# Optimization experiments

Measured on AMD Instinct MI355X. Metric: run time of the kernel, lower is better.

The kernel has to match this reference:

```python
import jax, jax.numpy as jnp
import numpy as np


def setup_inputs() -> dict:
    key = jax.random.key(0)
    ks = jax.random.split(key, 7)
    B, T, DIN, D = 64, 512, 512, 512
    s_in = 1.0 / np.sqrt(DIN)  # ~glorot-ish scale for input kernels
    s_h = 1.0 / np.sqrt(D)     # scale for recurrent kernels (orthogonal-ish magnitude)
    return {
        "X": jax.random.normal(ks[0], (B, T, DIN), jnp.float32),
        "W_z": jax.random.normal(ks[1], (DIN, D), jnp.float32) * s_in,
        "U_z": jax.random.normal(ks[2], (D, D), jnp.float32) * s_h,
        "b_z": jnp.zeros((D,), jnp.float32),
        "W_r": jax.random.normal(ks[3], (DIN, D), jnp.float32) * s_in,
        "U_r": jax.random.normal(ks[4], (D, D), jnp.float32) * s_h,
        "b_r": jnp.zeros((D,), jnp.float32),
        "W_h": jax.random.normal(ks[5], (DIN, D), jnp.float32) * s_in,
        "U_h": jax.random.normal(ks[6], (D, D), jnp.float32) * s_h,
        "b_h": jnp.zeros((D,), jnp.float32),
        "mask": jnp.ones((B, T), jnp.int32),
    }


def reference(X, W_z, U_z, b_z, W_r, U_r, b_r, W_h, U_h, b_h, mask):
    # X: [B, T, DIN] -> time-major [T, B, DIN]
    Xt = jnp.transpose(X, (1, 0, 2))
    # Precompute input projections (large GEMMs, done once): [T, B, D]
    xz = Xt @ W_z + b_z
    xr = Xt @ W_r + b_r
    xh = Xt @ W_h + b_h
    # Padded/shifted mask (pad=1): step t sees mask[t-1]; step 0 sees 0,
    # which zeroes the (zero) initial state exactly as in the theano code.
    m = jnp.transpose(mask, (1, 0)).astype(X.dtype)[:, :, None]  # [T, B, 1]
    m_tm1 = jnp.concatenate([jnp.zeros_like(m[:1]), m[:-1]], axis=0)

    B = X.shape[0]
    D = W_z.shape[1]
    h0 = jnp.zeros((B, D), X.dtype)

    def step(h_tm1, inputs):
        xz_t, xr_t, xh_t, mt = inputs
        hm = mt * h_tm1                                  # masked previous state
        z = jax.nn.sigmoid(xz_t + hm @ U_z)              # update gate
        r = jax.nn.sigmoid(xr_t + hm @ U_r)              # reset gate
        hh = jnp.tanh(xh_t + (r * hm) @ U_h)             # candidate
        h_t = z * hm + (1.0 - z) * hh
        return h_t, None

    h_last, _ = jax.lax.scan(step, h0, (xz, xr, xh, m_tm1))
    # return_sequences=False -> last hidden state [B, D]
    return h_last
```

## Files before the change

kernel.cpp:

```cpp
#include <hip/hip_runtime.h>
#include <hip/hip_fp16.h>

#define B_   64
#define T_   512
#define DINc 512
#define D_   512
#define NWG  16
#define JS   32

typedef _Float16 half8 __attribute__((ext_vector_type(8)));
typedef _Float16 half4 __attribute__((ext_vector_type(4)));
typedef float   floatx4 __attribute__((ext_vector_type(4)));
typedef unsigned uintx4 __attribute__((ext_vector_type(4)));

__global__ __launch_bounds__(256) void k_cvtX(const float* __restrict__ X, _Float16* __restrict__ Xh) {
    int idx = blockIdx.x * 256 + threadIdx.x;
    int m  = idx >> 6;
    int k8 = idx & 63;
    int b = m & 63, t = m >> 6;
    const float* src = X + ((size_t)(b * T_ + t)) * DINc + k8 * 8;
    float4 f0 = *(const float4*)(src);
    float4 f1 = *(const float4*)(src + 4);
    half8 h;
    h[0] = (_Float16)f0.x; h[1] = (_Float16)f0.y; h[2] = (_Float16)f0.z; h[3] = (_Float16)f0.w;
    h[4] = (_Float16)f1.x; h[5] = (_Float16)f1.y; h[6] = (_Float16)f1.z; h[7] = (_Float16)f1.w;
    *(half8*)(Xh + (size_t)m * DINc + k8 * 8) = h;
}

__global__ __launch_bounds__(256) void k_cvtW(const float* __restrict__ M0, const float* __restrict__ M1,
                                              const float* __restrict__ M2, _Float16* __restrict__ Mt) {
    __shared__ float tile[64][65];
    int g = blockIdx.z;
    const float* W = (g == 0) ? M0 : ((g == 1) ? M1 : M2);
    int n0 = blockIdx.x * 64, k0 = blockIdx.y * 64;
    int c = threadIdx.x & 63, r4 = threadIdx.x >> 6;
#pragma unroll
    for (int i = 0; i < 16; ++i) {
        int k = r4 + i * 4;
        tile[k][c] = W[(size_t)(k0 + k) * D_ + n0 + c];
    }
    __syncthreads();
    _Float16* out = Mt + (size_t)g * D_ * DINc;
#pragma unroll
    for (int i = 0; i < 16; ++i) {
        int n = r4 + i * 4;
        out[(size_t)(n0 + n) * DINc + k0 + c] = (_Float16)tile[c][n];
    }
}

__global__ __launch_bounds__(256) void k_cvtM(const int* __restrict__ mask, float* __restrict__ maskT) {
    int idx = blockIdx.x * 256 + threadIdx.x;
    int t = idx >> 6, b = idx & 63;
    maskT[idx] = (float)mask[(size_t)b * T_ + t];
}

__global__ __launch_bounds__(256) void k_gemm(const _Float16* __restrict__ Xh, const _Float16* __restrict__ Wt,
                                              const float* __restrict__ bz, const float* __restrict__ br,
                                              const float* __restrict__ bh, _Float16* __restrict__ xprojT) {
    __shared__ _Float16 As[128 * 32];
    __shared__ _Float16 Bs[128 * 32];
    int g = blockIdx.z;
    const _Float16* Wg = Wt + (size_t)g * 512 * 512;
    const float* bias = (g == 0) ? bz : ((g == 1) ? br : bh);
    _Float16* out = xprojT + (size_t)g * 16777216;
    int mb = blockIdx.x * 128, nb = blockIdx.y * 128;
    int tid = threadIdx.x, l = tid & 63, w = tid >> 6;
    int wr = w >> 1, wc = w & 1;
    int lr = l & 15, lg = l >> 4;

    floatx4 acc[4][4] = {};

    int ga0 = tid, ga1 = tid + 256;
    int ra0 = ga0 >> 2, ca0 = (ga0 & 3) * 8;
    int ra1 = ga1 >> 2, ca1 = (ga1 & 3) * 8;

    uint4 pa0, pa1, pb0, pb1;
    pa0 = *(const uint4*)(Xh + (size_t)(mb + ra0) * 512 + ca0);
    pa1 = *(const uint4*)(Xh + (size_t)(mb + ra1) * 512 + ca1);
    pb0 = *(const uint4*)(Wg + (size_t)(nb + ra0) * 512 + ca0);
    pb1 = *(const uint4*)(Wg + (size_t)(nb + ra1) * 512 + ca1);

    for (int kt = 0; kt < 16; ++kt) {
        __syncthreads();
        *(uint4*)(&As[ga0 * 8]) = pa0;
        *(uint4*)(&As[ga1 * 8]) = pa1;
        *(uint4*)(&Bs[ga0 * 8]) = pb0;
        *(uint4*)(&Bs[ga1 * 8]) = pb1;
        __syncthreads();
        if (kt < 15) {
            int kb = (kt + 1) * 32;
            pa0 = *(const uint4*)(Xh + (size_t)(mb + ra0) * 512 + kb + ca0);
            pa1 = *(const uint4*)(Xh + (size_t)(mb + ra1) * 512 + kb + ca1);
            pb0 = *(const uint4*)(Wg + (size_t)(nb + ra0) * 512 + kb + ca0);
            pb1 = *(const uint4*)(Wg + (size_t)(nb + ra1) * 512 + kb + ca1);
        }
        half8 af[4], bf[4];
#pragma unroll
        for (int mi = 0; mi < 4; mi++) af[mi] = *(const half8*)(&As[(wr * 64 + mi * 16 + lr) * 32 + lg * 8]);
#pragma unroll
        for (int ni = 0; ni < 4; ni++) bf[ni] = *(const half8*)(&Bs[(wc * 64 + ni * 16 + lr) * 32 + lg * 8]);
#pragma unroll
        for (int mi = 0; mi < 4; mi++)
#pragma unroll
            for (int ni = 0; ni < 4; ni++)
                acc[mi][ni] = __builtin_amdgcn_mfma_f32_16x16x32_f16(af[mi], bf[ni], acc[mi][ni], 0, 0, 0);
    }

#pragma unroll
    for (int ni = 0; ni < 4; ni++) {
        int col = nb + wc * 64 + ni * 16 + lr;
        float bv = bias[col];
#pragma unroll
        for (int mi = 0; mi < 4; mi++) {
            int row = mb + wr * 64 + mi * 16 + lg * 4;
            int tt = row >> 6, bb = row & 63;
            half4 hv;
#pragma unroll
            for (int i = 0; i < 4; i++) hv[i] = (_Float16)(acc[mi][ni][i] + bv);
            *(half4*)(out + (size_t)tt * 32768 + (size_t)col * 64 + bb) = hv;
        }
    }
}

__device__ __forceinline__ void st_agent(unsigned long long* p, unsigned long long v) {
    __hip_atomic_store(p, v, __ATOMIC_RELAXED, __HIP_MEMORY_SCOPE_AGENT);
}
__device__ __forceinline__ unsigned ld_flag(const unsigned* p) {
    return __hip_atomic_load(p, __ATOMIC_RELAXED, __HIP_MEMORY_SCOPE_AGENT);
}
__device__ __forceinline__ void st_flag(unsigned* p, unsigned v) {
    __hip_atomic_store(p, v, __ATOMIC_RELAXED, __HIP_MEMORY_SCOPE_AGENT);
}
__device__ __forceinline__ uintx4 ld16_agent(const void* p) {
    uintx4 r;
    asm volatile("global_load_dwordx4 %0, %1, off sc0 sc1" : "=v"(r) : "v"(p) : "memory");
    return r;
}

__device__ __forceinline__ unsigned long long pack_quad(const float v4[4], int lr) {
    unsigned long long unit = 0;
    int j = lr & 3;
#pragma unroll
    for (int i = 0; i < 4; i++) {
        _Float16 hv = (_Float16)v4[i];
        unsigned int v = (unsigned int)__builtin_bit_cast(unsigned short, hv);
        unsigned int o1 = __shfl_xor(v, 1, 64);
        unsigned int pair = (lr & 1) ? (o1 | (v << 16)) : (v | (o1 << 16));
        unsigned int q2 = __shfl_xor(pair, 2, 64);
        unsigned long long u = (lr & 2) ? ((unsigned long long)q2 | ((unsigned long long)pair << 32))
                                        : ((unsigned long long)pair | ((unsigned long long)q2 << 32));
        if (i == j) unit = u;
    }
    return unit;
}

__global__ __launch_bounds__(512, 2) void k_scan(const _Float16* __restrict__ Ut,
                                                 const float* __restrict__ maskT,
                                                 const _Float16* __restrict__ xprojT,
                                                 unsigned long long* __restrict__ hbuf,
                                                 unsigned long long* __restrict__ rhbuf,
                                                 unsigned* __restrict__ fh, unsigned* __restrict__ fr,
                                                 float* __restrict__ out) {
    __shared__ __align__(16) _Float16 Ulds[2 * JS * 512];
    __shared__ __align__(16) _Float16 Stg[64 * 512];
    char* StgB = (char*)Stg;
    int tid = threadIdx.x, l = tid & 63, w = tid >> 6;
    int lr = l & 15, lg = l >> 4;
    int mt = w >> 1, nt = w & 1;
    int slot = blockIdx.x;
    int jsb = slot * JS;

    for (int c = tid; c < 2 * JS * 64; c += 512) {
        int g  = c >> 11;
        int n  = (c >> 6) & 31;
        int k16 = c & 63;
        uintx4 v = *(const uintx4*)(Ut + (size_t)g * 262144 + (size_t)(jsb + n) * 512 + k16 * 8);
        *(uintx4*)((char*)Ulds + g * 32768 + n * 1024 + ((k16 * 16) ^ ((n & 7) << 4))) = v;
    }
    half8 uhf[16];
    {
        const _Float16* UtH = Ut + (size_t)2 * 262144;
        int ncol = jsb + nt * 16 + lr;
#pragma unroll
        for (int j = 0; j < 16; j++)
            uhf[j] = *(const half8*)(UtH + (size_t)ncol * 512 + j * 32 + lg * 8);
    }
    __syncthreads();

    const char* UB = (const char*)Ulds + (nt * 16 + lr) * 1024;
    const int swz = (lr & 7) << 4;

    int row0 = mt * 16 + lg * 4;
    int colg = jsb + nt * 16 + lr;

    float h4[4]  = {0.f, 0.f, 0.f, 0.f};
    float hm4[4] = {0.f, 0.f, 0.f, 0.f};

    const int punit = (mt * 16 + lg * 4 + (lr & 3)) * 128 + ((jsb + nt * 16) >> 2) + ((lr >> 2) & 3);
    const char* SB = StgB + (mt * 16 + lr) * 1024;

    const _Float16* xzB = xprojT + (size_t)colg * 64 + row0;
    const _Float16* xrB = xzB + (size_t)16777216;
    const _Float16* xhB = xrB + (size_t)16777216;

    {
        half4 xz0 = *(const half4*)(xzB);
        half4 xh0 = *(const half4*)(xhB);
        float4 m0 = *(const float4*)(maskT + row0);
#pragma unroll
        for (int i = 0; i < 4; i++) {
            float z  = 1.f / (1.f + __expf(-(float)xz0[i]));
            float hh = tanhf((float)xh0[i]);
            h4[i]  = (1.f - z) * hh;
            hm4[i] = ((float)m0[i]) * h4[i];
        }
        st_agent(hbuf + punit, pack_quad(hm4, lr));
        asm volatile("s_waitcnt vmcnt(0)" ::: "memory");
        __syncthreads();
        if (tid == 0) st_flag(fh + slot * 16, 1u);
    }

    for (int t = 1; t < T_; ++t) {
        const char* hmG = (const char*)(hbuf + ((t - 1) & 1) * 8192);
        char*       rhG = (char*)(rhbuf + (t & 1) * 8192);
        unsigned long long* rhW = rhbuf + (t & 1) * 8192;
        unsigned long long* hW  = hbuf + (t & 1) * 8192;

        half4 xzp = *(const half4*)(xzB + (size_t)t * 32768);
        half4 xrp = *(const half4*)(xrB + (size_t)t * 32768);
        half4 xhp = *(const half4*)(xhB + (size_t)t * 32768);
        float4 mv = *(const float4*)(maskT + (size_t)t * 64 + row0);

        if (w == 0) {
            for (;;) {
                unsigned v = (l < NWG) ? ld_flag(fh + l * 16) : (unsigned)t;
                if (__all(v >= (unsigned)t)) break;
            }
        }
        __syncthreads();
        {
            uintx4 gg[8];
#pragma unroll
            for (int it = 0; it < 8; ++it)
                gg[it] = ld16_agent(hmG + (w * 8 + it) * 1024 + l * 16);
            asm volatile("s_waitcnt vmcnt(0)" ::: "memory");
#pragma unroll
            for (int it = 0; it < 8; ++it)
                *(uintx4*)(StgB + (w * 8 + it) * 1024 + ((l * 16) ^ (it << 4))) = gg[it];
        }
        __syncthreads();
        half8 af[16];
#pragma unroll
        for (int j = 0; j < 16; j++)
            af[j] = *(const half8*)(SB + ((j * 64 + lg * 16) ^ swz));
        floatx4 accz = {0.f, 0.f, 0.f, 0.f}, accr = {0.f, 0.f, 0.f, 0.f};
#pragma unroll
        for (int j = 0; j < 16; j++) {
            int boff = (j * 64 + lg * 16) ^ swz;
            half8 bz8 = *(const half8*)(UB + boff);
            half8 br8 = *(const half8*)(UB + 32768 + boff);
            accz = __builtin_amdgcn_mfma_f32_16x16x32_f16(af[j], bz8, accz, 0, 0, 0);
            accr = __builtin_amdgcn_mfma_f32_16x16x32_f16(af[j], br8, accr, 0, 0, 0);
        }
        float z4[4], rh4[4];
#pragma unroll
        for (int i = 0; i < 4; i++) {
            float zz = 1.f / (1.f + __expf(-((float)xzp[i] + accz[i])));
            float rr = 1.f / (1.f + __expf(-((float)xrp[i] + accr[i])));
            z4[i]  = zz;
            rh4[i] = rr * hm4[i];
        }
        st_agent(rhW + punit, pack_quad(rh4, lr));
        asm volatile("s_waitcnt vmcnt(0)" ::: "memory");
        __syncthreads();
        if (tid == 0) st_flag(fr + slot * 16, (unsigned)t);

        if (w == 0) {
            for (;;) {
                unsigned v = (l < NWG) ? ld_flag(fr + l * 16) : (unsigned)t;
                if (__all(v >= (unsigned)t)) break;
            }
        }
        __syncthreads();
        {
            uintx4 gg[8];
#pragma unroll
            for (int it = 0; it < 8; ++it)
                gg[it] = ld16_agent(rhG + (w * 8 + it) * 1024 + l * 16);
            asm volatile("s_waitcnt vmcnt(0)" ::: "memory");
#pragma unroll
            for (int it = 0; it < 8; ++it)
                *(uintx4*)(StgB + (w * 8 + it) * 1024 + ((l * 16) ^ (it << 4))) = gg[it];
        }
        __syncthreads();
        half8 af2[16];
#pragma unroll
        for (int j = 0; j < 16; j++)
            af2[j] = *(const half8*)(SB + ((j * 64 + lg * 16) ^ swz));
        floatx4 acch0 = {0.f, 0.f, 0.f, 0.f}, acch1 = {0.f, 0.f, 0.f, 0.f};
#pragma unroll
        for (int j = 0; j < 16; j += 2) {
            acch0 = __builtin_amdgcn_mfma_f32_16x16x32_f16(af2[j],     uhf[j],     acch0, 0, 0, 0);
            acch1 = __builtin_amdgcn_mfma_f32_16x16x32_f16(af2[j + 1], uhf[j + 1], acch1, 0, 0, 0);
        }
#pragma unroll
        for (int i = 0; i < 4; i++) {
            float hh = tanhf((float)xhp[i] + acch0[i] + acch1[i]);
            h4[i]  = z4[i] * hm4[i] + (1.f - z4[i]) * hh;
            hm4[i] = ((float)mv[i]) * h4[i];
        }
        st_agent(hW + punit, pack_quad(hm4, lr));
        asm volatile("s_waitcnt vmcnt(0)" ::: "memory");
        __syncthreads();
        if (tid == 0) st_flag(fh + slot * 16, (unsigned)(t + 1));
    }

#pragma unroll
    for (int i = 0; i < 4; i++)
        out[(size_t)(row0 + i) * 512 + colg] = h4[i];
}

extern "C" void kernel_launch(void* const* d_in, const int* in_sizes, int n_in,
                              void* d_out, int out_size, void* d_ws, size_t ws_size,
                              hipStream_t stream) {
    (void)in_sizes; (void)n_in; (void)out_size; (void)ws_size;
    const float* X  = (const float*)d_in[0];
    const float* Wz = (const float*)d_in[1];
    const float* Uz = (const float*)d_in[2];
    const float* bz = (const float*)d_in[3];
    const float* Wr = (const float*)d_in[4];
    const float* Ur = (const float*)d_in[5];
    const float* br = (const float*)d_in[6];
    const float* Wh = (const float*)d_in[7];
    const float* Uh = (const float*)d_in[8];
    const float* bh = (const float*)d_in[9];
    const int* mask = (const int*)d_in[10];
    float* out = (float*)d_out;

    char* ws = (char*)d_ws;
    unsigned* fh = (unsigned*)ws;
    unsigned* fr = (unsigned*)(ws + 1024);
    unsigned long long* hbuf  = (unsigned long long*)(ws + 8192);
    unsigned long long* rhbuf = (unsigned long long*)(ws + 8192 + 131072);
    _Float16* Xh     = (_Float16*)(ws + 8192 + 2 * 131072);
    _Float16* Wt     = (_Float16*)(ws + 8192 + 2 * 131072 + 33554432);
    _Float16* Ut     = (_Float16*)(ws + 8192 + 2 * 131072 + 33554432 + 1572864);
    _Float16* xprojT = (_Float16*)(ws + 8192 + 2 * 131072 + 33554432 + 2 * 1572864);
    float*    maskT  = (float*)(ws + 8192 + 2 * 131072 + 33554432 + 2 * 1572864 + 100663296);

    hipMemsetAsync(ws, 0, 8192, stream);
    hipLaunchKernelGGL(k_cvtX, dim3(8192), dim3(256), 0, stream, X, Xh);
    hipLaunchKernelGGL(k_cvtW, dim3(8, 8, 3), dim3(256), 0, stream, Wz, Wr, Wh, Wt);
    hipLaunchKernelGGL(k_cvtW, dim3(8, 8, 3), dim3(256), 0, stream, Uz, Ur, Uh, Ut);
    hipLaunchKernelGGL(k_cvtM, dim3(128), dim3(256), 0, stream, mask, maskT);
    hipLaunchKernelGGL(k_gemm, dim3(256, 4, 3), dim3(256), 0, stream, Xh, Wt, bz, br, bh, xprojT);
    hipLaunchKernelGGL(k_scan, dim3(NWG), dim3(512), 0, stream, Ut, maskT, xprojT,
                       hbuf, rhbuf, fh, fr, out);
}
```

Before: 4.307 ms.

## Halve scan workgroups to 8 with 64 columns each and split-K staging

```diff
diff --git a/kernel.cpp b/kernel.cpp
--- a/kernel.cpp
+++ b/kernel.cpp
@@ -5,13 +5,18 @@
 #define T_   512
 #define DINc 512
 #define D_   512
-#define NWG  16
-#define JS   32
+#define NWG  8
+#define JS   64
 
 typedef _Float16 half8 __attribute__((ext_vector_type(8)));
 typedef _Float16 half4 __attribute__((ext_vector_type(4)));
 typedef float   floatx4 __attribute__((ext_vector_type(4)));
 typedef unsigned uintx4 __attribute__((ext_vector_type(4)));
+
+#define WAITV(N) asm volatile("s_waitcnt vmcnt(" #N ")" ::: "memory")
+#define WAITL()  asm volatile("s_waitcnt lgkmcnt(0)" ::: "memory")
+#define SCB()    __builtin_amdgcn_sched_barrier(0)
+#define RBAR()   do { SCB(); __builtin_amdgcn_s_barrier(); SCB(); } while (0)
 
 __global__ __launch_bounds__(256) void k_cvtX(const float* __restrict__ X, _Float16* __restrict__ Xh) {
     int idx = blockIdx.x * 256 + threadIdx.x;
@@ -154,28 +159,30 @@
     return unit;
 }
 
-__global__ __launch_bounds__(512, 2) void k_scan(const _Float16* __restrict__ Ut,
-                                                 const float* __restrict__ maskT,
-                                                 const _Float16* __restrict__ xprojT,
-                                                 unsigned long long* __restrict__ hbuf,
-                                                 unsigned long long* __restrict__ rhbuf,
-                                                 unsigned* __restrict__ fh, unsigned* __restrict__ fr,
-                                                 float* __restrict__ out) {
-    __shared__ __align__(16) _Float16 Ulds[2 * JS * 512];
-    __shared__ __align__(16) _Float16 Stg[64 * 512];
-    char* StgB = (char*)Stg;
+__global__ __launch_bounds__(512) void k_scan(const _Float16* __restrict__ Ut,
+                                              const float* __restrict__ maskT,
+                                              const _Float16* __restrict__ xprojT,
+                                              unsigned long long* __restrict__ hbuf,
+                                              unsigned long long* __restrict__ rhbuf,
+                                              unsigned* __restrict__ fh, unsigned* __restrict__ fr,
+                                              float* __restrict__ out) {
+    __shared__ __align__(16) char Lds[163840];
+    char* LdsB = Lds;
+    char* StgB = Lds + 131072;
     int tid = threadIdx.x, l = tid & 63, w = tid >> 6;
     int lr = l & 15, lg = l >> 4;
-    int mt = w >> 1, nt = w & 1;
+    int nt  = w >> 1;
+    int mt2 = w & 1;
+    int m0 = mt2 * 16, m1 = m0 + 32;
     int slot = blockIdx.x;
     int jsb = slot * JS;
 
-    for (int c = tid; c < 2 * JS * 64; c += 512) {
-        int g  = c >> 11;
-        int n  = (c >> 6) & 31;
+    for (int c = tid; c < 2 * 64 * 64; c += 512) {
+        int g   = c >> 12;
+        int n   = (c >> 6) & 63;
         int k16 = c & 63;
         uintx4 v = *(const uintx4*)(Ut + (size_t)g * 262144 + (size_t)(jsb + n) * 512 + k16 * 8);
-        *(uintx4*)((char*)Ulds + g * 32768 + n * 1024 + ((k16 * 16) ^ ((n & 7) << 4))) = v;
+        *(uintx4*)(LdsB + g * 65536 + n * 1024 + ((k16 * 16) ^ ((n & 7) << 4))) = v;
     }
     half8 uhf[16];
     {
@@ -187,49 +194,63 @@
     }
     __syncthreads();
 
-    const char* UB = (const char*)Ulds + (nt * 16 + lr) * 1024;
+    const char* UBz = LdsB + (nt * 16 + lr) * 1024;
+    const char* UBr = UBz + 65536;
     const int swz = (lr & 7) << 4;
-
-    int row0 = mt * 16 + lg * 4;
+    const int r0s = (m0 + lr) * 512;
+    const int r1s = (m1 + lr) * 512;
+
     int colg = jsb + nt * 16 + lr;
-
-    float h4[4]  = {0.f, 0.f, 0.f, 0.f};
-    float hm4[4] = {0.f, 0.f, 0.f, 0.f};
-
-    const int punit = (mt * 16 + lg * 4 + (lr & 3)) * 128 + ((jsb + nt * 16) >> 2) + ((lr >> 2) & 3);
-    const char* SB = StgB + (mt * 16 + lr) * 1024;
-
-    const _Float16* xzB = xprojT + (size_t)colg * 64 + row0;
+    int row0 = m0 + lg * 4;
+    int row1 = m1 + lg * 4;
+
+    float h4[2][4]  = {};
+    float hm4[2][4] = {};
+
+    const int punit0 = (m0 + lg * 4 + (lr & 3)) * 128 + ((jsb + nt * 16) >> 2) + ((lr >> 2) & 3);
+    const int punit1 = (m1 + lg * 4 + (lr & 3)) * 128 + ((jsb + nt * 16) >> 2) + ((lr >> 2) & 3);
+
+    const int gr0  = w * 8 + (l >> 5);
+    const int gcol = (l & 31) * 16;
+
+    const _Float16* xzB = xprojT + (size_t)colg * 64;
     const _Float16* xrB = xzB + (size_t)16777216;
     const _Float16* xhB = xrB + (size_t)16777216;
 
     {
-        half4 xz0 = *(const half4*)(xzB);
-        half4 xh0 = *(const half4*)(xhB);
-        float4 m0 = *(const float4*)(maskT + row0);
+        half4 xz0a = *(const half4*)(xzB + row0), xz0b = *(const half4*)(xzB + row1);
+        half4 xh0a = *(const half4*)(xhB + row0), xh0b = *(const half4*)(xhB + row1);
+        float4 m0a = *(const float4*)(maskT + row0), m0b = *(const float4*)(maskT + row1);
 #pragma unroll
         for (int i = 0; i < 4; i++) {
-            float z  = 1.f / (1.f + __expf(-(float)xz0[i]));
-            float hh = tanhf((float)xh0[i]);
-            h4[i]  = (1.f - z) * hh;
-            hm4[i] = ((float)m0[i]) * h4[i];
-        }
-        st_agent(hbuf + punit, pack_quad(hm4, lr));
-        asm volatile("s_waitcnt vmcnt(0)" ::: "memory");
+            float za = 1.f / (1.f + __expf(-(float)xz0a[i]));
+            float zb = 1.f / (1.f + __expf(-(float)xz0b[i]));
+            h4[0][i] = (1.f - za) * tanhf((float)xh0a[i]);
+            h4[1][i] = (1.f - zb) * tanhf((float)xh0b[i]);
+            hm4[0][i] = ((float)m0a[i]) * h4[0][i];
+            hm4[1][i] = ((float)m0b[i]) * h4[1][i];
+        }
+        st_agent(hbuf + punit0, pack_quad(hm4[0], lr));
+        st_agent(hbuf + punit1, pack_quad(hm4[1], lr));
+        WAITV(0);
         __syncthreads();
         if (tid == 0) st_flag(fh + slot * 16, 1u);
     }
 
     for (int t = 1; t < T_; ++t) {
         const char* hmG = (const char*)(hbuf + ((t - 1) & 1) * 8192);
-        char*       rhG = (char*)(rhbuf + (t & 1) * 8192);
+        const char* rhG = (const char*)(rhbuf + (t & 1) * 8192);
         unsigned long long* rhW = rhbuf + (t & 1) * 8192;
         unsigned long long* hW  = hbuf + (t & 1) * 8192;
 
-        half4 xzp = *(const half4*)(xzB + (size_t)t * 32768);
-        half4 xrp = *(const half4*)(xrB + (size_t)t * 32768);
-        half4 xhp = *(const half4*)(xhB + (size_t)t * 32768);
-        float4 mv = *(const float4*)(maskT + (size_t)t * 64 + row0);
+        const _Float16* xzT = xzB + (size_t)t * 32768;
+        const _Float16* xrT = xrB + (size_t)t * 32768;
+        const _Float16* xhT = xhB + (size_t)t * 32768;
+        half4 xzp0 = *(const half4*)(xzT + row0), xzp1 = *(const half4*)(xzT + row1);
+        half4 xrp0 = *(const half4*)(xrT + row0), xrp1 = *(const half4*)(xrT + row1);
+        half4 xhp0 = *(const half4*)(xhT + row0), xhp1 = *(const half4*)(xhT + row1);
+        float4 mva = *(const float4*)(maskT + (size_t)t * 64 + row0);
+        float4 mvb = *(const float4*)(maskT + (size_t)t * 64 + row1);
 
         if (w == 0) {
             for (;;) {
@@ -238,40 +259,69 @@
             }
         }
         __syncthreads();
+
+        floatx4 accz0 = {}, accz1 = {}, accr0 = {}, accr1 = {};
         {
             uintx4 gg[8];
 #pragma unroll
-            for (int it = 0; it < 8; ++it)
-                gg[it] = ld16_agent(hmG + (w * 8 + it) * 1024 + l * 16);
-            asm volatile("s_waitcnt vmcnt(0)" ::: "memory");
-#pragma unroll
-            for (int it = 0; it < 8; ++it)
-                *(uintx4*)(StgB + (w * 8 + it) * 1024 + ((l * 16) ^ (it << 4))) = gg[it];
-        }
-        __syncthreads();
-        half8 af[16];
-#pragma unroll
-        for (int j = 0; j < 16; j++)
-            af[j] = *(const half8*)(SB + ((j * 64 + lg * 16) ^ swz));
-        floatx4 accz = {0.f, 0.f, 0.f, 0.f}, accr = {0.f, 0.f, 0.f, 0.f};
-#pragma unroll
-        for (int j = 0; j < 16; j++) {
-            int boff = (j * 64 + lg * 16) ^ swz;
-            half8 bz8 = *(const half8*)(UB + boff);
-            half8 br8 = *(const half8*)(UB + 32768 + boff);
-            accz = __builtin_amdgcn_mfma_f32_16x16x32_f16(af[j], bz8, accz, 0, 0, 0);
-            accr = __builtin_amdgcn_mfma_f32_16x16x32_f16(af[j], br8, accr, 0, 0, 0);
-        }
-        float z4[4], rh4[4];
+            for (int it = 0; it < 4; ++it)
+                gg[it] = ld16_agent(hmG + (gr0 + it * 2) * 1024 + gcol);
+#pragma unroll
+            for (int it = 0; it < 4; ++it)
+                gg[4 + it] = ld16_agent(hmG + (gr0 + it * 2) * 1024 + 512 + gcol);
+            WAITV(4); SCB();
+#pragma unroll
+            for (int it = 0; it < 4; ++it) {
+                int r = gr0 + it * 2;
+                *(uintx4*)(StgB + r * 512 + (gcol ^ ((r & 7) << 4))) = gg[it];
+            }
+            WAITL(); RBAR();
+#pragma unroll
+            for (int j = 0; j < 8; ++j) {
+                int kbyte = j * 64 + lg * 16;
+                half8 a0 = *(const half8*)(StgB + r0s + (kbyte ^ swz));
+                half8 a1 = *(const half8*)(StgB + r1s + (kbyte ^ swz));
+                int ub = kbyte ^ swz;
+                half8 bz = *(const half8*)(UBz + ub);
+                half8 br = *(const half8*)(UBr + ub);
+                accz0 = __builtin_amdgcn_mfma_f32_16x16x32_f16(a0, bz, accz0, 0, 0, 0);
+                accr0 = __builtin_amdgcn_mfma_f32_16x16x32_f16(a0, br, accr0, 0, 0, 0);
+                accz1 = __builtin_amdgcn_mfma_f32_16x16x32_f16(a1, bz, accz1, 0, 0, 0);
+                accr1 = __builtin_amdgcn_mfma_f32_16x16x32_f16(a1, br, accr1, 0, 0, 0);
+            }
+            RBAR();
+            WAITV(0); SCB();
+#pragma unroll
+            for (int it = 0; it < 4; ++it) {
+                int r = gr0 + it * 2;
+                *(uintx4*)(StgB + r * 512 + (gcol ^ ((r & 7) << 4))) = gg[4 + it];
+            }
+            WAITL(); RBAR();
+#pragma unroll
+            for (int j = 0; j < 8; ++j) {
+                int kbyte = j * 64 + lg * 16;
+                half8 a0 = *(const half8*)(StgB + r0s + (kbyte ^ swz));
+                half8 a1 = *(const half8*)(StgB + r1s + (kbyte ^ swz));
+                int ub = (512 + kbyte) ^ swz;
+                half8 bz = *(const half8*)(UBz + ub);
+                half8 br = *(const half8*)(UBr + ub);
+                accz0 = __builtin_amdgcn_mfma_f32_16x16x32_f16(a0, bz, accz0, 0, 0, 0);
+                accr0 = __builtin_amdgcn_mfma_f32_16x16x32_f16(a0, br, accr0, 0, 0, 0);
+                accz1 = __builtin_amdgcn_mfma_f32_16x16x32_f16(a1, bz, accz1, 0, 0, 0);
+                accr1 = __builtin_amdgcn_mfma_f32_16x16x32_f16(a1, br, accr1, 0, 0, 0);
+            }
+        }
+        float z4[2][4], rh4[2][4];
 #pragma unroll
         for (int i = 0; i < 4; i++) {
-            float zz = 1.f / (1.f + __expf(-((float)xzp[i] + accz[i])));
-            float rr = 1.f / (1.f + __expf(-((float)xrp[i] + accr[i])));
-            z4[i]  = zz;
-            rh4[i] = rr * hm4[i];
-        }
-        st_agent(rhW + punit, pack_quad(rh4, lr));
-        asm volatile("s_waitcnt vmcnt(0)" ::: "memory");
+            z4[0][i] = 1.f / (1.f + __expf(-((float)xzp0[i] + accz0[i])));
+            z4[1][i] = 1.f / (1.f + __expf(-((float)xzp1[i] + accz1[i])));
+            rh4[0][i] = (1.f / (1.f + __expf(-((float)xrp0[i] + accr0[i])))) * hm4[0][i];
+            rh4[1][i] = (1.f / (1.f + __expf(-((float)xrp1[i] + accr1[i])))) * hm4[1][i];
+        }
+        st_agent(rhW + punit0, pack_quad(rh4[0], lr));
+        st_agent(rhW + punit1, pack_quad(rh4[1], lr));
+        WAITV(0);
         __syncthreads();
         if (tid == 0) st_flag(fr + slot * 16, (unsigned)t);
 
@@ -282,42 +332,69 @@
             }
         }
         __syncthreads();
+
+        floatx4 acch0 = {}, acch1 = {};
         {
             uintx4 gg[8];
 #pragma unroll
-            for (int it = 0; it < 8; ++it)
-                gg[it] = ld16_agent(rhG + (w * 8 + it) * 1024 + l * 16);
-            asm volatile("s_waitcnt vmcnt(0)" ::: "memory");
-#pragma unroll
-            for (int it = 0; it < 8; ++it)
-                *(uintx4*)(StgB + (w * 8 + it) * 1024 + ((l * 16) ^ (it << 4))) = gg[it];
-        }
-        __syncthreads();
-        half8 af2[16];
-#pragma unroll
-        for (int j = 0; j < 16; j++)
-            af2[j] = *(const half8*)(SB + ((j * 64 + lg * 16) ^ swz));
-        floatx4 acch0 = {0.f, 0.f, 0.f, 0.f}, acch1 = {0.f, 0.f, 0.f, 0.f};
-#pragma unroll
-        for (int j = 0; j < 16; j += 2) {
-            acch0 = __builtin_amdgcn_mfma_f32_16x16x32_f16(af2[j],     uhf[j],     acch0, 0, 0, 0);
-            acch1 = __builtin_amdgcn_mfma_f32_16x16x32_f16(af2[j + 1], uhf[j + 1], acch1, 0, 0, 0);
+            for (int it = 0; it < 4; ++it)
+                gg[it] = ld16_agent(rhG + (gr0 + it * 2) * 1024 + gcol);
+#pragma unroll
+            for (int it = 0; it < 4; ++it)
+                gg[4 + it] = ld16_agent(rhG + (gr0 + it * 2) * 1024 + 512 + gcol);
+            WAITV(4); SCB();
+#pragma unroll
+            for (int it = 0; it < 4; ++it) {
+                int r = gr0 + it * 2;
+                *(uintx4*)(StgB + r * 512 + (gcol ^ ((r & 7) << 4))) = gg[it];
+            }
+            WAITL(); RBAR();
+#pragma unroll
+            for (int j = 0; j < 8; ++j) {
+                int kbyte = j * 64 + lg * 16;
+                half8 a0 = *(const half8*)(StgB + r0s + (kbyte ^ swz));
+                half8 a1 = *(const half8*)(StgB + r1s + (kbyte ^ swz));
+                acch0 = __builtin_amdgcn_mfma_f32_16x16x32_f16(a0, uhf[j], acch0, 0, 0, 0);
+                acch1 = __builtin_amdgcn_mfma_f32_16x16x32_f16(a1, uhf[j], acch1, 0, 0, 0);
+            }
+            RBAR();
+            WAITV(0); SCB();
+#pragma unroll
+            for (int it = 0; it < 4; ++it) {
+                int r = gr0 + it * 2;
+                *(uintx4*)(StgB + r * 512 + (gcol ^ ((r & 7) << 4))) = gg[4 + it];
+            }
+            WAITL(); RBAR();
+#pragma unroll
+            for (int j = 0; j < 8; ++j) {
+                int kbyte = j * 64 + lg * 16;
+                half8 a0 = *(const half8*)(StgB + r0s + (kbyte ^ swz));
+                half8 a1 = *(const half8*)(StgB + r1s + (kbyte ^ swz));
+                acch0 = __builtin_amdgcn_mfma_f32_16x16x32_f16(a0, uhf[8 + j], acch0, 0, 0, 0);
+                acch1 = __builtin_amdgcn_mfma_f32_16x16x32_f16(a1, uhf[8 + j], acch1, 0, 0, 0);
+            }
         }
 #pragma unroll
         for (int i = 0; i < 4; i++) {
-            float hh = tanhf((float)xhp[i] + acch0[i] + acch1[i]);
-            h4[i]  = z4[i] * hm4[i] + (1.f - z4[i]) * hh;
-            hm4[i] = ((float)mv[i]) * h4[i];
-        }
-        st_agent(hW + punit, pack_quad(hm4, lr));
-        asm volatile("s_waitcnt vmcnt(0)" ::: "memory");
+            float hha = tanhf((float)xhp0[i] + acch0[i]);
+            float hhb = tanhf((float)xhp1[i] + acch1[i]);
+            h4[0][i] = z4[0][i] * hm4[0][i] + (1.f - z4[0][i]) * hha;
+            h4[1][i] = z4[1][i] * hm4[1][i] + (1.f - z4[1][i]) * hhb;
+            hm4[0][i] = ((float)mva[i]) * h4[0][i];
+            hm4[1][i] = ((float)mvb[i]) * h4[1][i];
+        }
+        st_agent(hW + punit0, pack_quad(hm4[0], lr));
+        st_agent(hW + punit1, pack_quad(hm4[1], lr));
+        WAITV(0);
         __syncthreads();
         if (tid == 0) st_flag(fh + slot * 16, (unsigned)(t + 1));
     }
 
 #pragma unroll
-    for (int i = 0; i < 4; i++)
-        out[(size_t)(row0 + i) * 512 + colg] = h4[i];
+    for (int i = 0; i < 4; i++) {
+        out[(size_t)(row0 + i) * 512 + colg] = h4[0][i];
+        out[(size_t)(row1 + i) * 512 + colg] = h4[1][i];
+    }
 }
 
 extern "C" void kernel_launch(void* const* d_in, const int* in_sizes, int n_in,
```

New measurement: 6.797 ms. 57.8% more time.

## Replace flag-based grid barriers with poisoned-data polling for inter-workgroup sync

Applied to the files above, without the earlier changes.

```diff
diff --git a/kernel.cpp b/kernel.cpp
--- a/kernel.cpp
+++ b/kernel.cpp
@@ -12,6 +12,9 @@
 typedef _Float16 half4 __attribute__((ext_vector_type(4)));
 typedef float   floatx4 __attribute__((ext_vector_type(4)));
 typedef unsigned uintx4 __attribute__((ext_vector_type(4)));
+
+#define WAITV0() asm volatile("s_waitcnt vmcnt(0)" ::: "memory")
+#define SCB()    __builtin_amdgcn_sched_barrier(0)
 
 __global__ __launch_bounds__(256) void k_cvtX(const float* __restrict__ X, _Float16* __restrict__ Xh) {
     int idx = blockIdx.x * 256 + threadIdx.x;
@@ -125,16 +128,13 @@
 __device__ __forceinline__ void st_agent(unsigned long long* p, unsigned long long v) {
     __hip_atomic_store(p, v, __ATOMIC_RELAXED, __HIP_MEMORY_SCOPE_AGENT);
 }
-__device__ __forceinline__ unsigned ld_flag(const unsigned* p) {
-    return __hip_atomic_load(p, __ATOMIC_RELAXED, __HIP_MEMORY_SCOPE_AGENT);
-}
-__device__ __forceinline__ void st_flag(unsigned* p, unsigned v) {
-    __hip_atomic_store(p, v, __ATOMIC_RELAXED, __HIP_MEMORY_SCOPE_AGENT);
-}
 __device__ __forceinline__ uintx4 ld16_agent(const void* p) {
     uintx4 r;
     asm volatile("global_load_dwordx4 %0, %1, off sc0 sc1" : "=v"(r) : "v"(p) : "memory");
     return r;
+}
+__device__ __forceinline__ bool chunk_valid(uintx4 v) {
+    return ((v[0] & v[1]) != 0xFFFFFFFFu) && ((v[2] & v[3]) != 0xFFFFFFFFu);
 }
 
 __device__ __forceinline__ unsigned long long pack_quad(const float v4[4], int lr) {
@@ -159,7 +159,6 @@
                                                  const _Float16* __restrict__ xprojT,
                                                  unsigned long long* __restrict__ hbuf,
                                                  unsigned long long* __restrict__ rhbuf,
-                                                 unsigned* __restrict__ fh, unsigned* __restrict__ fr,
                                                  float* __restrict__ out) {
     __shared__ __align__(16) _Float16 Ulds[2 * JS * 512];
     __shared__ __align__(16) _Float16 Stg[64 * 512];
@@ -215,39 +214,37 @@
             hm4[i] = ((float)m0[i]) * h4[i];
         }
         st_agent(hbuf + punit, pack_quad(hm4, lr));
-        asm volatile("s_waitcnt vmcnt(0)" ::: "memory");
-        __syncthreads();
-        if (tid == 0) st_flag(fh + slot * 16, 1u);
     }
 
     for (int t = 1; t < T_; ++t) {
         const char* hmG = (const char*)(hbuf + ((t - 1) & 1) * 8192);
-        char*       rhG = (char*)(rhbuf + (t & 1) * 8192);
-        unsigned long long* rhW = rhbuf + (t & 1) * 8192;
-        unsigned long long* hW  = hbuf + (t & 1) * 8192;
+        unsigned long long* rhPsn = rhbuf + ((t - 1) & 1) * 8192;
+        unsigned long long* hPsn  = hbuf  + ((t - 1) & 1) * 8192;
+        unsigned long long* rhW   = rhbuf + (t & 1) * 8192;
+        unsigned long long* hW    = hbuf  + (t & 1) * 8192;
+        const char* rhG = (const char*)rhW;
 
         half4 xzp = *(const half4*)(xzB + (size_t)t * 32768);
         half4 xrp = *(const half4*)(xrB + (size_t)t * 32768);
         half4 xhp = *(const half4*)(xhB + (size_t)t * 32768);
         float4 mv = *(const float4*)(maskT + (size_t)t * 64 + row0);
 
-        if (w == 0) {
-            for (;;) {
-                unsigned v = (l < NWG) ? ld_flag(fh + l * 16) : (unsigned)t;
-                if (__all(v >= (unsigned)t)) break;
-            }
-        }
-        __syncthreads();
-        {
-            uintx4 gg[8];
+        uintx4 gg[8];
+        for (;;) {
 #pragma unroll
             for (int it = 0; it < 8; ++it)
                 gg[it] = ld16_agent(hmG + (w * 8 + it) * 1024 + l * 16);
-            asm volatile("s_waitcnt vmcnt(0)" ::: "memory");
-#pragma unroll
-            for (int it = 0; it < 8; ++it)
-                *(uintx4*)(StgB + (w * 8 + it) * 1024 + ((l * 16) ^ (it << 4))) = gg[it];
-        }
+            WAITV0(); SCB();
+            bool ok = true;
+#pragma unroll
+            for (int it = 0; it < 8; ++it) ok = ok && chunk_valid(gg[it]);
+            if (__all(ok)) break;
+        }
+        st_agent(rhPsn + punit, ~0ull);
+        __syncthreads();
+#pragma unroll
+        for (int it = 0; it < 8; ++it)
+            *(uintx4*)(StgB + (w * 8 + it) * 1024 + ((l * 16) ^ (it << 4))) = gg[it];
         __syncthreads();
         half8 af[16];
 #pragma unroll
@@ -271,27 +268,23 @@
             rh4[i] = rr * hm4[i];
         }
         st_agent(rhW + punit, pack_quad(rh4, lr));
-        asm volatile("s_waitcnt vmcnt(0)" ::: "memory");
-        __syncthreads();
-        if (tid == 0) st_flag(fr + slot * 16, (unsigned)t);
-
-        if (w == 0) {
-            for (;;) {
-                unsigned v = (l < NWG) ? ld_flag(fr + l * 16) : (unsigned)t;
-                if (__all(v >= (unsigned)t)) break;
-            }
-        }
-        __syncthreads();
-        {
-            uintx4 gg[8];
+
+        uintx4 gg2[8];
+        for (;;) {
 #pragma unroll
             for (int it = 0; it < 8; ++it)
-                gg[it] = ld16_agent(rhG + (w * 8 + it) * 1024 + l * 16);
-            asm volatile("s_waitcnt vmcnt(0)" ::: "memory");
-#pragma unroll
-            for (int it = 0; it < 8; ++it)
-                *(uintx4*)(StgB + (w * 8 + it) * 1024 + ((l * 16) ^ (it << 4))) = gg[it];
-        }
+                gg2[it] = ld16_agent(rhG + (w * 8 + it) * 1024 + l * 16);
+            WAITV0(); SCB();
+            bool ok = true;
+#pragma unroll
+            for (int it = 0; it < 8; ++it) ok = ok && chunk_valid(gg2[it]);
+            if (__all(ok)) break;
+        }
+        st_agent(hPsn + punit, ~0ull);
+        __syncthreads();
+#pragma unroll
+        for (int it = 0; it < 8; ++it)
+            *(uintx4*)(StgB + (w * 8 + it) * 1024 + ((l * 16) ^ (it << 4))) = gg2[it];
         __syncthreads();
         half8 af2[16];
 #pragma unroll
@@ -310,9 +303,6 @@
             hm4[i] = ((float)mv[i]) * h4[i];
         }
         st_agent(hW + punit, pack_quad(hm4, lr));
-        asm volatile("s_waitcnt vmcnt(0)" ::: "memory");
-        __syncthreads();
-        if (tid == 0) st_flag(fh + slot * 16, (unsigned)(t + 1));
     }
 
 #pragma unroll
@@ -338,8 +328,6 @@
     float* out = (float*)d_out;
 
     char* ws = (char*)d_ws;
-    unsigned* fh = (unsigned*)ws;
-    unsigned* fr = (unsigned*)(ws + 1024);
     unsigned long long* hbuf  = (unsigned long long*)(ws + 8192);
     unsigned long long* rhbuf = (unsigned long long*)(ws + 8192 + 131072);
     _Float16* Xh     = (_Float16*)(ws + 8192 + 2 * 131072);
@@ -348,12 +336,12 @@
     _Float16* xprojT = (_Float16*)(ws + 8192 + 2 * 131072 + 33554432 + 2 * 1572864);
     float*    maskT  = (float*)(ws + 8192 + 2 * 131072 + 33554432 + 2 * 1572864 + 100663296);
 
-    hipMemsetAsync(ws, 0, 8192, stream);
+    hipMemsetAsync(ws + 8192, 0xFF, 2 * 131072, stream);
     hipLaunchKernelGGL(k_cvtX, dim3(8192), dim3(256), 0, stream, X, Xh);
     hipLaunchKernelGGL(k_cvtW, dim3(8, 8, 3), dim3(256), 0, stream, Wz, Wr, Wh, Wt);
     hipLaunchKernelGGL(k_cvtW, dim3(8, 8, 3), dim3(256), 0, stream, Uz, Ur, Uh, Ut);
     hipLaunchKernelGGL(k_cvtM, dim3(128), dim3(256), 0, stream, mask, maskT);
     hipLaunchKernelGGL(k_gemm, dim3(256, 4, 3), dim3(256), 0, stream, Xh, Wt, bz, br, bh, xprojT);
     hipLaunchKernelGGL(k_scan, dim3(NWG), dim3(512), 0, stream, Ut, maskT, xprojT,
-                       hbuf, rhbuf, fh, fr, out);
-}
+                       hbuf, rhbuf, out);
+}
```

Result: slower. 5.138 ms (+19.3%).

## Use per-wave flags, publish reset gate before update gate, split staging waits

Applied to the files above, without the earlier changes.

```diff
diff --git a/kernel.cpp b/kernel.cpp
--- a/kernel.cpp
+++ b/kernel.cpp
@@ -12,6 +12,9 @@
 typedef _Float16 half4 __attribute__((ext_vector_type(4)));
 typedef float   floatx4 __attribute__((ext_vector_type(4)));
 typedef unsigned uintx4 __attribute__((ext_vector_type(4)));
+
+#define WAITV(N) asm volatile("s_waitcnt vmcnt(" #N ")" ::: "memory")
+#define SCB()    __builtin_amdgcn_sched_barrier(0)
 
 __global__ __launch_bounds__(256) void k_cvtX(const float* __restrict__ X, _Float16* __restrict__ Xh) {
     int idx = blockIdx.x * 256 + threadIdx.x;
@@ -154,13 +157,22 @@
     return unit;
 }
 
-__global__ __launch_bounds__(512, 2) void k_scan(const _Float16* __restrict__ Ut,
-                                                 const float* __restrict__ maskT,
-                                                 const _Float16* __restrict__ xprojT,
-                                                 unsigned long long* __restrict__ hbuf,
-                                                 unsigned long long* __restrict__ rhbuf,
-                                                 unsigned* __restrict__ fh, unsigned* __restrict__ fr,
-                                                 float* __restrict__ out) {
+__device__ __forceinline__ void poll_flags(const unsigned* f, unsigned need, int l) {
+    for (;;) {
+        unsigned v0 = ld_flag(f + l * 16);
+        unsigned v1 = ld_flag(f + (64 + l) * 16);
+        if (__all(v0 >= need && v1 >= need)) break;
+    }
+    SCB();
+}
+
+__global__ __launch_bounds__(512) void k_scan(const _Float16* __restrict__ Ut,
+                                              const float* __restrict__ maskT,
+                                              const _Float16* __restrict__ xprojT,
+                                              unsigned long long* __restrict__ hbuf,
+                                              unsigned long long* __restrict__ rhbuf,
+                                              unsigned* __restrict__ fh, unsigned* __restrict__ fr,
+                                              float* __restrict__ out) {
     __shared__ __align__(16) _Float16 Ulds[2 * JS * 512];
     __shared__ __align__(16) _Float16 Stg[64 * 512];
     char* StgB = (char*)Stg;
@@ -169,6 +181,7 @@
     int mt = w >> 1, nt = w & 1;
     int slot = blockIdx.x;
     int jsb = slot * JS;
+    const int fidx = slot * 8 + w;
 
     for (int c = tid; c < 2 * JS * 64; c += 512) {
         int g  = c >> 11;
@@ -209,43 +222,41 @@
         float4 m0 = *(const float4*)(maskT + row0);
 #pragma unroll
         for (int i = 0; i < 4; i++) {
-            float z  = 1.f / (1.f + __expf(-(float)xz0[i]));
+            float z  = __builtin_amdgcn_rcpf(1.f + __expf(-(float)xz0[i]));
             float hh = tanhf((float)xh0[i]);
             h4[i]  = (1.f - z) * hh;
             hm4[i] = ((float)m0[i]) * h4[i];
         }
         st_agent(hbuf + punit, pack_quad(hm4, lr));
-        asm volatile("s_waitcnt vmcnt(0)" ::: "memory");
-        __syncthreads();
-        if (tid == 0) st_flag(fh + slot * 16, 1u);
+        WAITV(0);
+        if (l == 0) st_flag(fh + fidx * 16, 1u);
     }
 
     for (int t = 1; t < T_; ++t) {
         const char* hmG = (const char*)(hbuf + ((t - 1) & 1) * 8192);
-        char*       rhG = (char*)(rhbuf + (t & 1) * 8192);
         unsigned long long* rhW = rhbuf + (t & 1) * 8192;
-        unsigned long long* hW  = hbuf + (t & 1) * 8192;
+        unsigned long long* hW  = hbuf  + (t & 1) * 8192;
+        const char* rhG = (const char*)rhW;
 
         half4 xzp = *(const half4*)(xzB + (size_t)t * 32768);
         half4 xrp = *(const half4*)(xrB + (size_t)t * 32768);
         half4 xhp = *(const half4*)(xhB + (size_t)t * 32768);
         float4 mv = *(const float4*)(maskT + (size_t)t * 64 + row0);
 
-        if (w == 0) {
-            for (;;) {
-                unsigned v = (l < NWG) ? ld_flag(fh + l * 16) : (unsigned)t;
-                if (__all(v >= (unsigned)t)) break;
-            }
-        }
-        __syncthreads();
+        __syncthreads();
+        poll_flags(fh, (unsigned)t, l);
         {
             uintx4 gg[8];
 #pragma unroll
             for (int it = 0; it < 8; ++it)
                 gg[it] = ld16_agent(hmG + (w * 8 + it) * 1024 + l * 16);
-            asm volatile("s_waitcnt vmcnt(0)" ::: "memory");
-#pragma unroll
-            for (int it = 0; it < 8; ++it)
+            WAITV(4); SCB();
+#pragma unroll
+            for (int it = 0; it < 4; ++it)
+                *(uintx4*)(StgB + (w * 8 + it) * 1024 + ((l * 16) ^ (it << 4))) = gg[it];
+            WAITV(0); SCB();
+#pragma unroll
+            for (int it = 4; it < 8; ++it)
                 *(uintx4*)(StgB + (w * 8 + it) * 1024 + ((l * 16) ^ (it << 4))) = gg[it];
         }
         __syncthreads();
@@ -253,43 +264,48 @@
 #pragma unroll
         for (int j = 0; j < 16; j++)
             af[j] = *(const half8*)(SB + ((j * 64 + lg * 16) ^ swz));
-        floatx4 accz = {0.f, 0.f, 0.f, 0.f}, accr = {0.f, 0.f, 0.f, 0.f};
+        floatx4 accr = {0.f, 0.f, 0.f, 0.f};
+#pragma unroll
+        for (int j = 0; j < 16; j++) {
+            int boff = (j * 64 + lg * 16) ^ swz;
+            half8 br8 = *(const half8*)(UB + 32768 + boff);
+            accr = __builtin_amdgcn_mfma_f32_16x16x32_f16(af[j], br8, accr, 0, 0, 0);
+        }
+        float rh4[4];
+#pragma unroll
+        for (int i = 0; i < 4; i++) {
+            float rr = __builtin_amdgcn_rcpf(1.f + __expf(-((float)xrp[i] + accr[i])));
+            rh4[i] = rr * hm4[i];
+        }
+        st_agent(rhW + punit, pack_quad(rh4, lr));
+        WAITV(0);
+        if (l == 0) st_flag(fr + fidx * 16, (unsigned)t);
+        floatx4 accz = {0.f, 0.f, 0.f, 0.f};
 #pragma unroll
         for (int j = 0; j < 16; j++) {
             int boff = (j * 64 + lg * 16) ^ swz;
             half8 bz8 = *(const half8*)(UB + boff);
-            half8 br8 = *(const half8*)(UB + 32768 + boff);
             accz = __builtin_amdgcn_mfma_f32_16x16x32_f16(af[j], bz8, accz, 0, 0, 0);
-            accr = __builtin_amdgcn_mfma_f32_16x16x32_f16(af[j], br8, accr, 0, 0, 0);
-        }
-        float z4[4], rh4[4];
-#pragma unroll
-        for (int i = 0; i < 4; i++) {
-            float zz = 1.f / (1.f + __expf(-((float)xzp[i] + accz[i])));
-            float rr = 1.f / (1.f + __expf(-((float)xrp[i] + accr[i])));
-            z4[i]  = zz;
-            rh4[i] = rr * hm4[i];
-        }
-        st_agent(rhW + punit, pack_quad(rh4, lr));
-        asm volatile("s_waitcnt vmcnt(0)" ::: "memory");
-        __syncthreads();
-        if (tid == 0) st_flag(fr + slot * 16, (unsigned)t);
-
-        if (w == 0) {
-            for (;;) {
-                unsigned v = (l < NWG) ? ld_flag(fr + l * 16) : (unsigned)t;
-                if (__all(v >= (unsigned)t)) break;
-            }
-        }
-        __syncthreads();
+        }
+        float z4[4];
+#pragma unroll
+        for (int i = 0; i < 4; i++)
+            z4[i] = __builtin_amdgcn_rcpf(1.f + __expf(-((float)xzp[i] + accz[i])));
+
+        __syncthreads();
+        poll_flags(fr, (unsigned)t, l);
         {
             uintx4 gg[8];
 #pragma unroll
             for (int it = 0; it < 8; ++it)
                 gg[it] = ld16_agent(rhG + (w * 8 + it) * 1024 + l * 16);
-            asm volatile("s_waitcnt vmcnt(0)" ::: "memory");
-#pragma unroll
-            for (int it = 0; it < 8; ++it)
+            WAITV(4); SCB();
+#pragma unroll
+            for (int it = 0; it < 4; ++it)
+                *(uintx4*)(StgB + (w * 8 + it) * 1024 + ((l * 16) ^ (it << 4))) = gg[it];
+            WAITV(0); SCB();
+#pragma unroll
+            for (int it = 4; it < 8; ++it)
                 *(uintx4*)(StgB + (w * 8 + it) * 1024 + ((l * 16) ^ (it << 4))) = gg[it];
         }
         __syncthreads();
@@ -310,9 +326,8 @@
             hm4[i] = ((float)mv[i]) * h4[i];
         }
         st_agent(hW + punit, pack_quad(hm4, lr));
-        asm volatile("s_waitcnt vmcnt(0)" ::: "memory");
-        __syncthreads();
-        if (tid == 0) st_flag(fh + slot * 16, (unsigned)(t + 1));
+        WAITV(0);
+        if (l == 0) st_flag(fh + fidx * 16, (unsigned)(t + 1));
     }
 
 #pragma unroll
@@ -339,16 +354,16 @@
 
     char* ws = (char*)d_ws;
     unsigned* fh = (unsigned*)ws;
-    unsigned* fr = (unsigned*)(ws + 1024);
-    unsigned long long* hbuf  = (unsigned long long*)(ws + 8192);
-    unsigned long long* rhbuf = (unsigned long long*)(ws + 8192 + 131072);
-    _Float16* Xh     = (_Float16*)(ws + 8192 + 2 * 131072);
-    _Float16* Wt     = (_Float16*)(ws + 8192 + 2 * 131072 + 33554432);
-    _Float16* Ut     = (_Float16*)(ws + 8192 + 2 * 131072 + 33554432 + 1572864);
-    _Float16* xprojT = (_Float16*)(ws + 8192 + 2 * 131072 + 33554432 + 2 * 1572864);
-    float*    maskT  = (float*)(ws + 8192 + 2 * 131072 + 33554432 + 2 * 1572864 + 100663296);
-
-    hipMemsetAsync(ws, 0, 8192, stream);
+    unsigned* fr = (unsigned*)(ws + 8192);
+    unsigned long long* hbuf  = (unsigned long long*)(ws + 16384);
+    unsigned long long* rhbuf = (unsigned long long*)(ws + 16384 + 131072);
+    _Float16* Xh     = (_Float16*)(ws + 16384 + 2 * 131072);
+    _Float16* Wt     = (_Float16*)(ws + 16384 + 2 * 131072 + 33554432);
+    _Float16* Ut     = (_Float16*)(ws + 16384 + 2 * 131072 + 33554432 + 1572864);
+    _Float16* xprojT = (_Float16*)(ws + 16384 + 2 * 131072 + 33554432 + 2 * 1572864);
+    float*    maskT  = (float*)(ws + 16384 + 2 * 131072 + 33554432 + 2 * 1572864 + 100663296);
+
+    hipMemsetAsync(ws, 0, 16384, stream);
     hipLaunchKernelGGL(k_cvtX, dim3(8192), dim3(256), 0, stream, X, Xh);
     hipLaunchKernelGGL(k_cvtW, dim3(8, 8, 3), dim3(256), 0, stream, Wz, Wr, Wh, Wt);
     hipLaunchKernelGGL(k_cvtW, dim3(8, 8, 3), dim3(256), 0, stream, Uz, Ur, Uh, Ut);
```

Measured after the change: 3.764 ms, median of 2. -12.6%, faster.
